# Kernel optimization log

Measured on AMD Instinct MI355X. Metric: run time of the kernel, lower is better.

The kernel has to match this reference:

```python
import jax, jax.numpy as jnp
import numpy as np

N, E, D = 50000, 300000, 64
EPS = 0.0  # eps buffer, train_eps=False


def setup_inputs() -> dict:
    key = jax.random.key(0)
    ks = jax.random.split(key, 24)
    inp = {}
    i = 0
    for d in range(3):
        inp[f"x{d}"] = jax.random.normal(ks[i], (N, D), jnp.float32); i += 1
        inp[f"up_index{d}"] = jax.random.randint(ks[i], (2, E), 0, N, jnp.int32); i += 1
        inp[f"down_index{d}"] = jax.random.randint(ks[i], (2, E), 0, N, jnp.int32); i += 1
        inp[f"up_attr{d}"] = jax.random.normal(ks[i], (E, D), jnp.float32); i += 1
        inp[f"down_attr{d}"] = jax.random.normal(ks[i], (E, D), jnp.float32); i += 1
    s2 = 1.0 / np.sqrt(2 * D)
    s1 = 1.0 / np.sqrt(D)
    inp["W_up"] = jax.random.normal(ks[i], (2 * D, D), jnp.float32) * s2; i += 1
    inp["b_up"] = jnp.zeros((D,), jnp.float32)
    inp["W_down"] = jax.random.normal(ks[i], (2 * D, D), jnp.float32) * s2; i += 1
    inp["b_down"] = jnp.zeros((D,), jnp.float32)
    inp["W1"] = jax.random.normal(ks[i], (D, D), jnp.float32) * s1; i += 1
    inp["b1"] = jnp.zeros((D,), jnp.float32)
    inp["W2"] = jax.random.normal(ks[i], (D, D), jnp.float32) * s1; i += 1
    inp["b2"] = jnp.zeros((D,), jnp.float32)
    return inp


def _level(x, up_idx, down_idx, up_attr, down_attr,
           W_up, b_up, W_down, b_down, W1, b1, W2, b2):
    # message_up: gather source feats, concat attr, MLP, scatter-add to targets
    m_up = jax.nn.relu(jnp.concatenate([x[up_idx[1]], up_attr], axis=-1) @ W_up + b_up)
    out_up = jax.ops.segment_sum(m_up, up_idx[0], num_segments=N)
    m_dn = jax.nn.relu(jnp.concatenate([x[down_idx[1]], down_attr], axis=-1) @ W_down + b_down)
    out_dn = jax.ops.segment_sum(m_dn, down_idx[0], num_segments=N)
    # out_up += (1+eps)x; out_down += (1+eps)x; update(out_up + out_down)
    h = out_up + out_dn + (2.0 * (1.0 + EPS)) * x
    return jax.nn.relu(jax.nn.relu(h @ W1 + b1) @ W2 + b2)


def reference(x0, up_index0, down_index0, up_attr0, down_attr0,
              x1, up_index1, down_index1, up_attr1, down_attr1,
              x2, up_index2, down_index2, up_attr2, down_attr2,
              W_up, b_up, W_down, b_down, W1, b1, W2, b2):
    params = (W_up, b_up, W_down, b_down, W1, b1, W2, b2)
    o0 = _level(x0, up_index0, down_index0, up_attr0, down_attr0, *params)
    o1 = _level(x1, up_index1, down_index1, up_attr1, down_attr1, *params)
    o2 = _level(x2, up_index2, down_index2, up_attr2, down_attr2, *params)
    return (o0, o1, o2)
```

## Files before the change

### kernel.cpp

```cpp
#include <hip/hip_runtime.h>
#include <hip/hip_fp16.h>

#define NN 50000
#define NE 300000
#define ETILES (NE / 16)
#define NTILES (NN / 16)

typedef _Float16 f16;
typedef _Float16 f16x4 __attribute__((ext_vector_type(4)));
typedef _Float16 f16x8 __attribute__((ext_vector_type(8)));
typedef float f32x4 __attribute__((ext_vector_type(4)));

__device__ __forceinline__ f16x4 cvt4(float4 v) {
    f16x4 r; r.x = (f16)v.x; r.y = (f16)v.y; r.z = (f16)v.z; r.w = (f16)v.w;
    return r;
}

__global__ void init2_kernel(const float* __restrict__ x0, const float* __restrict__ x1,
                             const float* __restrict__ x2,
                             f16* __restrict__ hbase, f16* __restrict__ xhbase) {
    const size_t i = (size_t)blockIdx.x * 256 + threadIdx.x;
    const int lvl = (int)(i / (NN * 16));
    const size_t li = i - (size_t)lvl * (NN * 16);
    const float* xs = (lvl == 0) ? x0 : (lvl == 1) ? x1 : x2;
    float4 v = ((const float4*)xs)[li];
    f16x4 xo, ho;
    xo.x = (f16)v.x;        xo.y = (f16)v.y;        xo.z = (f16)v.z;        xo.w = (f16)v.w;
    ho.x = (f16)(2.f*v.x);  ho.y = (f16)(2.f*v.y);  ho.z = (f16)(2.f*v.z);  ho.w = (f16)(2.f*v.w);
    ((f16x4*)(xhbase + (size_t)lvl * NN * 64))[li] = xo;
    ((f16x4*)(hbase  + (size_t)lvl * NN * 64))[li] = ho;
}

__global__ void initf32_kernel(const float* __restrict__ x0, const float* __restrict__ x1,
                               const float* __restrict__ x2, float* __restrict__ hbase) {
    const size_t i = (size_t)blockIdx.x * 256 + threadIdx.x;
    const int lvl = (int)(i / (NN * 16));
    const size_t li = i - (size_t)lvl * (NN * 16);
    const float* xs = (lvl == 0) ? x0 : (lvl == 1) ? x1 : x2;
    float4 v = ((const float4*)xs)[li];
    ((float4*)(hbase + (size_t)lvl * NN * 64))[li] =
        make_float4(2.f * v.x, 2.f * v.y, 2.f * v.z, 2.f * v.w);
}

__global__ void wtrans_kernel(const float* __restrict__ WU, const float* __restrict__ WD,
                              f16* __restrict__ WtU, f16* __restrict__ WtD) {
    const int i = blockIdx.x * 256 + threadIdx.x;
    const int k = i >> 6, c = i & 63;
    WtU[c * 128 + k] = (f16)WU[i];
    WtD[c * 128 + k] = (f16)WD[i];
}

#define WLDS_STRIDE 136

__device__ __forceinline__ int ld_comb(const int* __restrict__ idx, int tile, int l5) {
    const int e0 = tile << 4;
    return idx[(l5 < 16) ? (NE + e0 + l5) : (e0 + l5 - 16)];
}

__global__ __launch_bounds__(256) void edge4_kernel(
    const f16* __restrict__ xh,
    const int* __restrict__ ui, const int* __restrict__ di,
    const float* __restrict__ ua, const float* __restrict__ da,
    const f16* __restrict__ WtU, const f16* __restrict__ WtD,
    const float* __restrict__ bU, const float* __restrict__ bD,
    __half* __restrict__ h) {

    __shared__ __align__(16) f16 Wlds[64 * WLDS_STRIDE];

    const int dir = blockIdx.y;
    const int* __restrict__ idx    = dir ? di : ui;
    const float* __restrict__ attr = dir ? da : ua;
    const f16* __restrict__ Wt     = dir ? WtD : WtU;
    const float* __restrict__ b    = dir ? bD : bU;

    const int tt   = threadIdx.x;
    const int lane = tt & 63;
    const int wid  = tt >> 6;
    const int lr   = lane & 15;
    const int lg   = (lane >> 4) & 3;
    const int l5   = lane & 31;

    for (int i = tt; i < 1024; i += 256) {
        const int row = i >> 4, seg = i & 15;
        *(f16x8*)&Wlds[row * WLDS_STRIDE + seg * 8] = *(const f16x8*)&Wt[row * 128 + seg * 8];
    }
    float bf[4];
#pragma unroll
    for (int n = 0; n < 4; ++n) bf[n] = b[n * 16 + lr];
    __syncthreads();

    const float4* a4 = (const float4*)attr;

    const int S = gridDim.x * 4;
    int t = blockIdx.x * 4 + wid;
    if (t >= ETILES) return;

    int cB;
    int srcT, tgT[4];
    f16x4 gx[4];
    float4 pA[4];
    {
        const int cA = ld_comb(idx, t, l5);
        const int tn1 = t + S;
        cB = ld_comb(idx, (tn1 < ETILES) ? tn1 : t, l5);
        srcT = __shfl(cA, lr);
#pragma unroll
        for (int j = 0; j < 4; ++j) tgT[j] = __shfl(cA, 16 + 4 * lg + j);
        const int e0 = t << 4;
#pragma unroll
        for (int k0 = 0; k0 < 4; ++k0)
            gx[k0] = *(const f16x4*)&xh[(size_t)srcT * 64 + k0 * 16 + 4 * lg];
#pragma unroll
        for (int k0 = 0; k0 < 4; ++k0)
            pA[k0] = a4[(size_t)(e0 + lr) * 16 + 4 * k0 + lg];
    }

    for (; t < ETILES; t += S) {
        const int tn  = t + S;
        const int tnn = tn + S;

        const int srcN = __shfl(cB, lr);
        int tgN[4];
#pragma unroll
        for (int j = 0; j < 4; ++j) tgN[j] = __shfl(cB, 16 + 4 * lg + j);
        const int cC = ld_comb(idx, (tnn < ETILES) ? tnn : t, l5);

        const int tnc   = (tn < ETILES) ? tn : t;
        const int srcNc = (tn < ETILES) ? srcN : srcT;
        f16x4 gxN[4];
        float4 pAN[4];
        {
            const int e0n = tnc << 4;
#pragma unroll
            for (int k0 = 0; k0 < 4; ++k0)
                gxN[k0] = *(const f16x4*)&xh[(size_t)srcNc * 64 + k0 * 16 + 4 * lg];
#pragma unroll
            for (int k0 = 0; k0 < 4; ++k0)
                pAN[k0] = a4[(size_t)(e0n + lr) * 16 + 4 * k0 + lg];
        }

        f16x4 afr[8];
#pragma unroll
        for (int k0 = 0; k0 < 4; ++k0) afr[k0] = gx[k0];
#pragma unroll
        for (int k0 = 0; k0 < 4; ++k0) afr[4 + k0] = cvt4(pA[k0]);

        f32x4 acc[4];
#pragma unroll
        for (int n = 0; n < 4; ++n) acc[n] = (f32x4){0.f, 0.f, 0.f, 0.f};
#pragma unroll
        for (int k0 = 0; k0 < 8; ++k0) {
#pragma unroll
            for (int n = 0; n < 4; ++n) {
                const f16x4 wf = *(const f16x4*)&Wlds[(n * 16 + lr) * WLDS_STRIDE + k0 * 16 + 4 * lg];
                acc[n] = __builtin_amdgcn_mfma_f32_16x16x16f16(afr[k0], wf, acc[n], 0, 0, 0);
            }
        }

#pragma unroll
        for (int j = 0; j < 4; ++j) {
            float v[4], vn[4];
#pragma unroll
            for (int n = 0; n < 4; ++n) v[n] = fmaxf(acc[n][j] + bf[n], 0.f);
#pragma unroll
            for (int n = 0; n < 4; ++n) vn[n] = __shfl_xor(v[n], 1);
            __half* hp = h + (size_t)tgT[j] * 64;
            if ((lane & 1) == 0) {
                unsafeAtomicAdd((__half2*)(hp + 0 * 16 + lr), __floats2half2_rn(v[0], vn[0]));
                unsafeAtomicAdd((__half2*)(hp + 1 * 16 + lr), __floats2half2_rn(v[1], vn[1]));
            } else {
                unsafeAtomicAdd((__half2*)(hp + 2 * 16 + lr - 1), __floats2half2_rn(vn[2], v[2]));
                unsafeAtomicAdd((__half2*)(hp + 3 * 16 + lr - 1), __floats2half2_rn(vn[3], v[3]));
            }
        }

        srcT = srcN;
#pragma unroll
        for (int j = 0; j < 4; ++j) tgT[j] = tgN[j];
#pragma unroll
        for (int k0 = 0; k0 < 4; ++k0) { gx[k0] = gxN[k0]; pA[k0] = pAN[k0]; }
        cB = cC;
    }
}

__global__ __launch_bounds__(256) void edge_f32_kernel(
    const float* __restrict__ x, const int* __restrict__ idx,
    const float* __restrict__ attr, const float* __restrict__ W,
    const float* __restrict__ b, float* __restrict__ h) {

    const int t    = threadIdx.x;
    const int lane = t & 63;
    const int wid  = t >> 6;
    const int lr   = lane & 15;
    const int lg   = (lane >> 4) & 3;

    f16x4 wf[8][4];
#pragma unroll
    for (int k0 = 0; k0 < 8; ++k0) {
        const int kb = k0 * 16 + 4 * lg;
#pragma unroll
        for (int n = 0; n < 4; ++n) {
            const int c = n * 16 + lr;
            f16x4 w;
            w.x = (f16)W[(kb + 0) * 64 + c];
            w.y = (f16)W[(kb + 1) * 64 + c];
            w.z = (f16)W[(kb + 2) * 64 + c];
            w.w = (f16)W[(kb + 3) * 64 + c];
            wf[k0][n] = w;
        }
    }
    float bf[4];
#pragma unroll
    for (int n = 0; n < 4; ++n) bf[n] = b[n * 16 + lr];

    const float4* x4 = (const float4*)x;
    const float4* a4 = (const float4*)attr;

    const int gw     = blockIdx.x * 4 + wid;
    const int stride = gridDim.x * 4;
    for (int tile = gw; tile < ETILES; tile += stride) {
        const int e0  = tile << 4;
        const int src = idx[NE + e0 + lr];
        int tg[4];
#pragma unroll
        for (int j = 0; j < 4; ++j) tg[j] = idx[e0 + 4 * lg + j];

        f16x4 a[8];
#pragma unroll
        for (int k0 = 0; k0 < 4; ++k0)
            a[k0] = cvt4(x4[(size_t)src * 16 + 4 * k0 + lg]);
#pragma unroll
        for (int k0 = 0; k0 < 4; ++k0)
            a[4 + k0] = cvt4(a4[(size_t)(e0 + lr) * 16 + 4 * k0 + lg]);

        f32x4 acc[4];
#pragma unroll
        for (int n = 0; n < 4; ++n) acc[n] = (f32x4){0.f, 0.f, 0.f, 0.f};
#pragma unroll
        for (int k0 = 0; k0 < 8; ++k0)
#pragma unroll
            for (int n = 0; n < 4; ++n)
                acc[n] = __builtin_amdgcn_mfma_f32_16x16x16f16(a[k0], wf[k0][n], acc[n], 0, 0, 0);

#pragma unroll
        for (int j = 0; j < 4; ++j) {
            float* hp = h + (size_t)tg[j] * 64;
#pragma unroll
            for (int n = 0; n < 4; ++n) {
                float v = fmaxf(acc[n][j] + bf[n], 0.f);
                unsafeAtomicAdd(hp + n * 16 + lr, v);
            }
        }
    }
}

template<bool HALF>
__global__ __launch_bounds__(256) void node_kernel(
    const void* __restrict__ hbase, float* __restrict__ outb,
    const float* __restrict__ W1, const float* __restrict__ b1,
    const float* __restrict__ W2, const float* __restrict__ b2) {

    __shared__ f16 Y[4][16 * 72];

    const int t    = threadIdx.x;
    const int lane = t & 63;
    const int wid  = t >> 6;
    const int lr   = lane & 15;
    const int lg   = (lane >> 4) & 3;

    f16x4 w1f[4][4], w2f[4][4];
#pragma unroll
    for (int k0 = 0; k0 < 4; ++k0) {
        const int kb = k0 * 16 + 4 * lg;
#pragma unroll
        for (int n = 0; n < 4; ++n) {
            const int c = n * 16 + lr;
            f16x4 w;
            w.x = (f16)W1[(kb + 0) * 64 + c];
            w.y = (f16)W1[(kb + 1) * 64 + c];
            w.z = (f16)W1[(kb + 2) * 64 + c];
            w.w = (f16)W1[(kb + 3) * 64 + c];
            w1f[k0][n] = w;
            w.x = (f16)W2[(kb + 0) * 64 + c];
            w.y = (f16)W2[(kb + 1) * 64 + c];
            w.z = (f16)W2[(kb + 2) * 64 + c];
            w.w = (f16)W2[(kb + 3) * 64 + c];
            w2f[k0][n] = w;
        }
    }
    float b1f[4], b2f[4];
#pragma unroll
    for (int n = 0; n < 4; ++n) {
        b1f[n] = b1[n * 16 + lr];
        b2f[n] = b2[n * 16 + lr];
    }

    const int gw     = blockIdx.x * 4 + wid;
    const int stride = gridDim.x * 4;
    for (int tile = gw; tile < 3 * NTILES; tile += stride) {
        const int lvl = tile / NTILES;
        const int n0  = (tile - lvl * NTILES) << 4;
        float* out = outb + (size_t)lvl * NN * 64;

        f16x4 a[4];
        if (HALF) {
            const f16* h16 = (const f16*)hbase + (size_t)lvl * NN * 64;
#pragma unroll
            for (int k0 = 0; k0 < 4; ++k0)
                a[k0] = *(const f16x4*)&h16[(size_t)(n0 + lr) * 64 + k0 * 16 + 4 * lg];
        } else {
            const float4* h4 = (const float4*)((const float*)hbase + (size_t)lvl * NN * 64);
#pragma unroll
            for (int k0 = 0; k0 < 4; ++k0)
                a[k0] = cvt4(h4[(size_t)(n0 + lr) * 16 + 4 * k0 + lg]);
        }

        f32x4 acc[4];
#pragma unroll
        for (int n = 0; n < 4; ++n) acc[n] = (f32x4){0.f, 0.f, 0.f, 0.f};
#pragma unroll
        for (int k0 = 0; k0 < 4; ++k0)
#pragma unroll
            for (int n = 0; n < 4; ++n)
                acc[n] = __builtin_amdgcn_mfma_f32_16x16x16f16(a[k0], w1f[k0][n], acc[n], 0, 0, 0);

#pragma unroll
        for (int n = 0; n < 4; ++n)
#pragma unroll
            for (int j = 0; j < 4; ++j) {
                float v = acc[n][j] + b1f[n];
                v = v > 0.f ? v : 0.f;
                Y[wid][(4 * lg + j) * 72 + n * 16 + lr] = (f16)v;
            }

        f16x4 a2[4];
#pragma unroll
        for (int k0 = 0; k0 < 4; ++k0)
            a2[k0] = *(const f16x4*)&Y[wid][lr * 72 + k0 * 16 + 4 * lg];

        f32x4 acc2[4];
#pragma unroll
        for (int n = 0; n < 4; ++n) acc2[n] = (f32x4){0.f, 0.f, 0.f, 0.f};
#pragma unroll
        for (int k0 = 0; k0 < 4; ++k0)
#pragma unroll
            for (int n = 0; n < 4; ++n)
                acc2[n] = __builtin_amdgcn_mfma_f32_16x16x16f16(a2[k0], w2f[k0][n], acc2[n], 0, 0, 0);

#pragma unroll
        for (int n = 0; n < 4; ++n)
#pragma unroll
            for (int j = 0; j < 4; ++j) {
                float v = acc2[n][j] + b2f[n];
                v = v > 0.f ? v : 0.f;
                out[(size_t)(n0 + 4 * lg + j) * 64 + n * 16 + lr] = v;
            }
    }
}

extern "C" void kernel_launch(void* const* d_in, const int* in_sizes, int n_in,
                              void* d_out, int out_size, void* d_ws, size_t ws_size,
                              hipStream_t stream) {
    (void)in_sizes; (void)n_in; (void)out_size;

    const float* W_up   = (const float*)d_in[15];
    const float* b_up   = (const float*)d_in[16];
    const float* W_down = (const float*)d_in[17];
    const float* b_down = (const float*)d_in[18];
    const float* W1     = (const float*)d_in[19];
    const float* b1     = (const float*)d_in[20];
    const float* W2     = (const float*)d_in[21];
    const float* b2     = (const float*)d_in[22];

    const float* x0 = (const float*)d_in[0];
    const float* x1 = (const float*)d_in[5];
    const float* x2 = (const float*)d_in[10];

    const size_t hbytes  = (size_t)3 * NN * 64 * sizeof(f16);
    const size_t need    = 2 * hbytes + (size_t)2 * 128 * 64 * sizeof(f16);

    if (ws_size >= need) {
        f16* hbase  = (f16*)d_ws;
        f16* xhbase = hbase + (size_t)3 * NN * 64;
        f16* WtU    = (f16*)((char*)d_ws + 2 * hbytes);
        f16* WtD    = WtU + 128 * 64;

        wtrans_kernel<<<32, 256, 0, stream>>>(W_up, W_down, WtU, WtD);
        init2_kernel<<<9375, 256, 0, stream>>>(x0, x1, x2, hbase, xhbase);
        for (int d = 0; d < 3; ++d) {
            const int*   ui = (const int*)  d_in[5 * d + 1];
            const int*   di = (const int*)  d_in[5 * d + 2];
            const float* ua = (const float*)d_in[5 * d + 3];
            const float* da = (const float*)d_in[5 * d + 4];
            const f16* xh = xhbase + (size_t)d * NN * 64;
            __half* h = (__half*)(hbase + (size_t)d * NN * 64);
            edge4_kernel<<<dim3(1024, 2), 256, 0, stream>>>(
                xh, ui, di, ua, da, WtU, WtD, b_up, b_down, h);
        }
        node_kernel<true><<<586, 256, 0, stream>>>(hbase, (float*)d_out, W1, b1, W2, b2);
    } else {
        float* hbase = (float*)d_out;
        initf32_kernel<<<9375, 256, 0, stream>>>(x0, x1, x2, hbase);
        for (int d = 0; d < 3; ++d) {
            const float* x  = (const float*)d_in[5 * d + 0];
            const int*   ui = (const int*)  d_in[5 * d + 1];
            const int*   di = (const int*)  d_in[5 * d + 2];
            const float* ua = (const float*)d_in[5 * d + 3];
            const float* da = (const float*)d_in[5 * d + 4];
            float* h = hbase + (size_t)d * NN * 64;
            edge_f32_kernel<<<1024, 256, 0, stream>>>(x, ui, ua, W_up,   b_up,   h);
            edge_f32_kernel<<<1024, 256, 0, stream>>>(x, di, da, W_down, b_down, h);
        }
        node_kernel<false><<<586, 256, 0, stream>>>(hbase, (float*)d_out, W1, b1, W2, b2);
    }
}
```

Before: 433.8 us.

## Bucket edges by target and fuse edge messages with node MLP in LDS

Adds a counting-sort pass (histogram, scan, scatter of edge ids) that groups edges into 128-node target buckets. A single fused kernel per bucket and level computes both up and down messages with MFMA, accumulates them with fp32 LDS atomics instead of global half2 atomics, and then applies the two-layer node MLP directly from LDS. This removes the global fp16 aggregation buffer round trip and the global atomic traffic, at the cost of extra sort kernels, indirect gathers of attr rows through edge ids, and possible load imbalance across buckets. The old fp32 fallback path is dropped and the old edge4 kernel loses its software prefetch.

```diff
diff --git a/kernel.cpp b/kernel.cpp
--- a/kernel.cpp
+++ b/kernel.cpp
@@ -5,15 +5,34 @@
 #define NE 300000
 #define ETILES (NE / 16)
 #define NTILES (NN / 16)
+#define WLDS_STRIDE 136
+#define BKT 128
+#define NB 391
+#define NB1 392
+#define NCH 74
+#define CHSZ 4096
+#define HSTR 68
 
 typedef _Float16 f16;
 typedef _Float16 f16x4 __attribute__((ext_vector_type(4)));
-typedef _Float16 f16x8 __attribute__((ext_vector_type(8)));
 typedef float f32x4 __attribute__((ext_vector_type(4)));
+
+struct Idx6 { const int* p[6]; };
+struct FA { const float* x[3]; const int* idx[6]; const float* attr[6]; };
 
 __device__ __forceinline__ f16x4 cvt4(float4 v) {
     f16x4 r; r.x = (f16)v.x; r.y = (f16)v.y; r.z = (f16)v.z; r.w = (f16)v.w;
     return r;
+}
+
+__global__ void init_xh_kernel(const float* __restrict__ x0, const float* __restrict__ x1,
+                               const float* __restrict__ x2, f16* __restrict__ xhbase) {
+    const size_t i = (size_t)blockIdx.x * 256 + threadIdx.x;
+    const int lvl = (int)(i / (NN * 16));
+    const size_t li = i - (size_t)lvl * (NN * 16);
+    const float* xs = (lvl == 0) ? x0 : (lvl == 1) ? x1 : x2;
+    float4 v = ((const float4*)xs)[li];
+    ((f16x4*)(xhbase + (size_t)lvl * NN * 64))[li] = cvt4(v);
 }
 
 __global__ void init2_kernel(const float* __restrict__ x0, const float* __restrict__ x1,
@@ -31,17 +50,6 @@
     ((f16x4*)(hbase  + (size_t)lvl * NN * 64))[li] = ho;
 }
 
-__global__ void initf32_kernel(const float* __restrict__ x0, const float* __restrict__ x1,
-                               const float* __restrict__ x2, float* __restrict__ hbase) {
-    const size_t i = (size_t)blockIdx.x * 256 + threadIdx.x;
-    const int lvl = (int)(i / (NN * 16));
-    const size_t li = i - (size_t)lvl * (NN * 16);
-    const float* xs = (lvl == 0) ? x0 : (lvl == 1) ? x1 : x2;
-    float4 v = ((const float4*)xs)[li];
-    ((float4*)(hbase + (size_t)lvl * NN * 64))[li] =
-        make_float4(2.f * v.x, 2.f * v.y, 2.f * v.z, 2.f * v.w);
-}
-
 __global__ void wtrans_kernel(const float* __restrict__ WU, const float* __restrict__ WD,
                               f16* __restrict__ WtU, f16* __restrict__ WtD) {
     const int i = blockIdx.x * 256 + threadIdx.x;
@@ -50,7 +58,260 @@
     WtD[c * 128 + k] = (f16)WD[i];
 }
 
-#define WLDS_STRIDE 136
+__global__ void w12trans_kernel(const float* __restrict__ W1, const float* __restrict__ W2,
+                                f16* __restrict__ W1t, f16* __restrict__ W2t) {
+    const int i = blockIdx.x * 256 + threadIdx.x;
+    const int k = i >> 6, c = i & 63;
+    W1t[c * 64 + k] = (f16)W1[i];
+    W2t[c * 64 + k] = (f16)W2[i];
+}
+
+__global__ void hist_b_kernel(Idx6 idx, int* __restrict__ cntBC) {
+    __shared__ int c[NB];
+    const int t = threadIdx.x, ch = blockIdx.x, d = blockIdx.y;
+    for (int i = t; i < NB; i += 256) c[i] = 0;
+    __syncthreads();
+    const int base = ch * CHSZ;
+    const int* tg = idx.p[d];
+#pragma unroll
+    for (int i = 0; i < 16; ++i) {
+        const int e = base + i * 256 + t;
+        if (e < NE) atomicAdd(&c[tg[e] >> 7], 1);
+    }
+    __syncthreads();
+    for (int i = t; i < NB; i += 256) cntBC[(d * NB + i) * NCH + ch] = c[i];
+}
+
+__global__ void scan_b_kernel(const int* __restrict__ cntBC, int* __restrict__ offBC,
+                              int* __restrict__ rowptrB) {
+    __shared__ int sb[512];
+    const int t = threadIdx.x, d = blockIdx.x;
+    int tot = 0;
+    if (t < NB)
+        for (int c = 0; c < NCH; ++c) tot += cntBC[(d * NB + t) * NCH + c];
+    sb[t] = tot; __syncthreads();
+#pragma unroll
+    for (int off = 1; off < 512; off <<= 1) {
+        int v = (t >= off) ? sb[t - off] : 0;
+        __syncthreads();
+        sb[t] += v;
+        __syncthreads();
+    }
+    const int excl = sb[t] - tot;
+    if (t < NB) {
+        rowptrB[d * NB1 + t] = excl;
+        int run = excl;
+        for (int c = 0; c < NCH; ++c) {
+            offBC[(d * NB + t) * NCH + c] = run;
+            run += cntBC[(d * NB + t) * NCH + c];
+        }
+        if (t == NB - 1) rowptrB[d * NB1 + NB] = run;
+    }
+}
+
+__global__ void write_eids_b_kernel(Idx6 idx, const int* __restrict__ offBC,
+                                    int* __restrict__ eids) {
+    __shared__ int cur[NB];
+    const int t = threadIdx.x, ch = blockIdx.x, d = blockIdx.y;
+    for (int i = t; i < NB; i += 256) cur[i] = offBC[(d * NB + i) * NCH + ch];
+    __syncthreads();
+    const int base = ch * CHSZ;
+    const int* tg = idx.p[d];
+#pragma unroll
+    for (int i = 0; i < 16; ++i) {
+        const int e = base + i * 256 + t;
+        if (e < NE) {
+            const int p = atomicAdd(&cur[tg[e] >> 7], 1);
+            eids[(size_t)d * NE + p] = e;
+        }
+    }
+}
+
+__global__ __launch_bounds__(512) void fused_kernel(
+    FA fa, const f16* __restrict__ xhbase,
+    const f16* __restrict__ WtU, const f16* __restrict__ WtD,
+    const float* __restrict__ bU, const float* __restrict__ bD,
+    const int* __restrict__ eids, const int* __restrict__ rowptrB,
+    const f16* __restrict__ W1t, const f16* __restrict__ W2t,
+    const float* __restrict__ b1, const float* __restrict__ b2,
+    float* __restrict__ outb) {
+
+    __shared__ float hl[BKT * HSTR];
+    __shared__ f16 Y[8][16 * 72];
+
+    const int lvl  = blockIdx.y;
+    const int bkt  = blockIdx.x;
+    const int base = bkt * BKT;
+    const int tid  = threadIdx.x;
+    const int lane = tid & 63;
+    const int w    = tid >> 6;
+    const int lr   = lane & 15;
+    const int lg   = (lane >> 4) & 3;
+
+    const float* x  = fa.x[lvl];
+    const f16*   xh = xhbase + (size_t)lvl * NN * 64;
+    float*       out = outb + (size_t)lvl * NN * 64;
+
+    for (int i = tid; i < BKT * 16; i += 512) {
+        const int nl = i >> 4, c4 = i & 15;
+        float4 v = make_float4(0.f, 0.f, 0.f, 0.f);
+        if (base + nl < NN) v = ((const float4*)x)[(size_t)(base + nl) * 16 + c4];
+        ((float4*)&hl[nl * HSTR])[c4] = make_float4(2.f*v.x, 2.f*v.y, 2.f*v.z, 2.f*v.w);
+    }
+    __syncthreads();
+
+    for (int dir = 0; dir < 2; ++dir) {
+        const int d = 2 * lvl + dir;
+        const int* __restrict__ gidx  = fa.idx[d];
+        const float4* __restrict__ a4 = (const float4*)fa.attr[d];
+        const f16* __restrict__ Wt    = dir ? WtD : WtU;
+        const float* __restrict__ bb  = dir ? bD : bU;
+        const int* __restrict__ eid   = eids + (size_t)d * NE;
+        const int s0 = rowptrB[d * NB1 + bkt];
+        const int s1 = rowptrB[d * NB1 + bkt + 1];
+        if (s1 <= s0) continue;
+        const int T = (s1 - s0 + 15) >> 4;
+
+        f16x4 wf[8][4];
+#pragma unroll
+        for (int k0 = 0; k0 < 8; ++k0)
+#pragma unroll
+            for (int n = 0; n < 4; ++n)
+                wf[k0][n] = *(const f16x4*)&Wt[(n * 16 + lr) * 128 + k0 * 16 + 4 * lg];
+        float bf[4];
+#pragma unroll
+        for (int n = 0; n < 4; ++n) bf[n] = bb[n * 16 + lr];
+
+        if (w < T) {
+            int eA, sA, gA, gB;
+            float4 aB[4]; f16x4 xB[4];
+            {
+                const int sb = s0 + w * 16;
+                const int sl = (sb + lr < s1 - 1) ? (sb + lr) : (s1 - 1);
+                eA = eid[sl]; sA = gidx[NE + eA]; gA = gidx[eA];
+            }
+            {
+#pragma unroll
+                for (int k0 = 0; k0 < 4; ++k0) aB[k0] = a4[(size_t)eA * 16 + 4 * k0 + lg];
+#pragma unroll
+                for (int k0 = 0; k0 < 4; ++k0)
+                    xB[k0] = *(const f16x4*)&xh[(size_t)sA * 64 + k0 * 16 + 4 * lg];
+                gB = gA;
+            }
+            {
+                const int t2 = (w + 8 < T) ? (w + 8) : w;
+                const int sb = s0 + t2 * 16;
+                const int sl = (sb + lr < s1 - 1) ? (sb + lr) : (s1 - 1);
+                eA = eid[sl]; sA = gidx[NE + eA]; gA = gidx[eA];
+            }
+            for (int t = w; t < T; t += 8) {
+                float4 aN[4]; f16x4 xN[4]; const int gN = gA;
+#pragma unroll
+                for (int k0 = 0; k0 < 4; ++k0) aN[k0] = a4[(size_t)eA * 16 + 4 * k0 + lg];
+#pragma unroll
+                for (int k0 = 0; k0 < 4; ++k0)
+                    xN[k0] = *(const f16x4*)&xh[(size_t)sA * 64 + k0 * 16 + 4 * lg];
+                {
+                    const int t2 = (t + 16 < T) ? (t + 16) : t;
+                    const int sb = s0 + t2 * 16;
+                    const int sl = (sb + lr < s1 - 1) ? (sb + lr) : (s1 - 1);
+                    eA = eid[sl]; sA = gidx[NE + eA]; gA = gidx[eA];
+                }
+                {
+                    const int sb = s0 + t * 16;
+                    f16x4 afr[8];
+#pragma unroll
+                    for (int k0 = 0; k0 < 4; ++k0) afr[k0] = xB[k0];
+#pragma unroll
+                    for (int k0 = 0; k0 < 4; ++k0) afr[4 + k0] = cvt4(aB[k0]);
+                    f32x4 acc[4];
+#pragma unroll
+                    for (int n = 0; n < 4; ++n) acc[n] = (f32x4){0.f, 0.f, 0.f, 0.f};
+#pragma unroll
+                    for (int k0 = 0; k0 < 8; ++k0)
+#pragma unroll
+                        for (int n = 0; n < 4; ++n)
+                            acc[n] = __builtin_amdgcn_mfma_f32_16x16x16f16(afr[k0], wf[k0][n], acc[n], 0, 0, 0);
+#pragma unroll
+                    for (int j = 0; j < 4; ++j) {
+                        const int row = 4 * lg + j;
+                        const int nl  = __shfl(gB, row) - base;
+                        const bool ok = (sb + row) < s1;
+#pragma unroll
+                        for (int n = 0; n < 4; ++n) {
+                            const float v = fmaxf(acc[n][j] + bf[n], 0.f);
+                            if (ok) atomicAdd(&hl[nl * HSTR + n * 16 + lr], v);
+                        }
+                    }
+                }
+#pragma unroll
+                for (int k0 = 0; k0 < 4; ++k0) { aB[k0] = aN[k0]; xB[k0] = xN[k0]; }
+                gB = gN;
+            }
+        }
+    }
+    __syncthreads();
+
+    f16x4 w1f[4][4], w2f[4][4];
+#pragma unroll
+    for (int k0 = 0; k0 < 4; ++k0)
+#pragma unroll
+        for (int n = 0; n < 4; ++n) {
+            w1f[k0][n] = *(const f16x4*)&W1t[(n * 16 + lr) * 64 + k0 * 16 + 4 * lg];
+            w2f[k0][n] = *(const f16x4*)&W2t[(n * 16 + lr) * 64 + k0 * 16 + 4 * lg];
+        }
+    float b1f[4], b2f[4];
+#pragma unroll
+    for (int n = 0; n < 4; ++n) { b1f[n] = b1[n * 16 + lr]; b2f[n] = b2[n * 16 + lr]; }
+
+    const int r0 = w * 16;
+    f16x4 a[4];
+#pragma unroll
+    for (int k0 = 0; k0 < 4; ++k0) {
+        f16x4 tv;
+#pragma unroll
+        for (int jj = 0; jj < 4; ++jj)
+            tv[jj] = (f16)hl[(r0 + lr) * HSTR + k0 * 16 + 4 * lg + jj];
+        a[k0] = tv;
+    }
+    f32x4 acc[4];
+#pragma unroll
+    for (int n = 0; n < 4; ++n) acc[n] = (f32x4){0.f, 0.f, 0.f, 0.f};
+#pragma unroll
+    for (int k0 = 0; k0 < 4; ++k0)
+#pragma unroll
+        for (int n = 0; n < 4; ++n)
+            acc[n] = __builtin_amdgcn_mfma_f32_16x16x16f16(a[k0], w1f[k0][n], acc[n], 0, 0, 0);
+#pragma unroll
+    for (int n = 0; n < 4; ++n)
+#pragma unroll
+        for (int j = 0; j < 4; ++j) {
+            float v = acc[n][j] + b1f[n];
+            v = v > 0.f ? v : 0.f;
+            Y[w][(4 * lg + j) * 72 + n * 16 + lr] = (f16)v;
+        }
+    f16x4 a2[4];
+#pragma unroll
+    for (int k0 = 0; k0 < 4; ++k0)
+        a2[k0] = *(const f16x4*)&Y[w][lr * 72 + k0 * 16 + 4 * lg];
+    f32x4 acc2[4];
+#pragma unroll
+    for (int n = 0; n < 4; ++n) acc2[n] = (f32x4){0.f, 0.f, 0.f, 0.f};
+#pragma unroll
+    for (int k0 = 0; k0 < 4; ++k0)
+#pragma unroll
+        for (int n = 0; n < 4; ++n)
+            acc2[n] = __builtin_amdgcn_mfma_f32_16x16x16f16(a2[k0], w2f[k0][n], acc2[n], 0, 0, 0);
+#pragma unroll
+    for (int n = 0; n < 4; ++n)
+#pragma unroll
+        for (int j = 0; j < 4; ++j) {
+            const int node = base + r0 + 4 * lg + j;
+            float v = acc2[n][j] + b2f[n];
+            v = v > 0.f ? v : 0.f;
+            if (node < NN) out[(size_t)node * 64 + n * 16 + lr] = v;
+        }
+}
 
 __device__ __forceinline__ int ld_comb(const int* __restrict__ idx, int tile, int l5) {
     const int e0 = tile << 4;
@@ -80,9 +341,9 @@
     const int lg   = (lane >> 4) & 3;
     const int l5   = lane & 31;
 
-    for (int i = tt; i < 1024; i += 256) {
-        const int row = i >> 4, seg = i & 15;
-        *(f16x8*)&Wlds[row * WLDS_STRIDE + seg * 8] = *(const f16x8*)&Wt[row * 128 + seg * 8];
+    for (int i = tt; i < 2048; i += 256) {
+        const int row = i >> 5, seg = i & 31;
+        *(f16x4*)&Wlds[row * WLDS_STRIDE + seg * 4] = *(const f16x4*)&Wt[row * 128 + seg * 4];
     }
     float bf[4];
 #pragma unroll
@@ -90,72 +351,36 @@
     __syncthreads();
 
     const float4* a4 = (const float4*)attr;
-
     const int S = gridDim.x * 4;
     int t = blockIdx.x * 4 + wid;
     if (t >= ETILES) return;
 
-    int cB;
-    int srcT, tgT[4];
-    f16x4 gx[4];
-    float4 pA[4];
-    {
+    for (; t < ETILES; t += S) {
+        const int e0 = t << 4;
         const int cA = ld_comb(idx, t, l5);
-        const int tn1 = t + S;
-        cB = ld_comb(idx, (tn1 < ETILES) ? tn1 : t, l5);
-        srcT = __shfl(cA, lr);
-#pragma unroll
-        for (int j = 0; j < 4; ++j) tgT[j] = __shfl(cA, 16 + 4 * lg + j);
-        const int e0 = t << 4;
+        const int src = __shfl(cA, lr);
+        int tg[4];
+#pragma unroll
+        for (int j = 0; j < 4; ++j) tg[j] = __shfl(cA, 16 + 4 * lg + j);
+
+        f16x4 afr[8];
 #pragma unroll
         for (int k0 = 0; k0 < 4; ++k0)
-            gx[k0] = *(const f16x4*)&xh[(size_t)srcT * 64 + k0 * 16 + 4 * lg];
+            afr[k0] = *(const f16x4*)&xh[(size_t)src * 64 + k0 * 16 + 4 * lg];
 #pragma unroll
         for (int k0 = 0; k0 < 4; ++k0)
-            pA[k0] = a4[(size_t)(e0 + lr) * 16 + 4 * k0 + lg];
-    }
-
-    for (; t < ETILES; t += S) {
-        const int tn  = t + S;
-        const int tnn = tn + S;
-
-        const int srcN = __shfl(cB, lr);
-        int tgN[4];
-#pragma unroll
-        for (int j = 0; j < 4; ++j) tgN[j] = __shfl(cB, 16 + 4 * lg + j);
-        const int cC = ld_comb(idx, (tnn < ETILES) ? tnn : t, l5);
-
-        const int tnc   = (tn < ETILES) ? tn : t;
-        const int srcNc = (tn < ETILES) ? srcN : srcT;
-        f16x4 gxN[4];
-        float4 pAN[4];
-        {
-            const int e0n = tnc << 4;
-#pragma unroll
-            for (int k0 = 0; k0 < 4; ++k0)
-                gxN[k0] = *(const f16x4*)&xh[(size_t)srcNc * 64 + k0 * 16 + 4 * lg];
-#pragma unroll
-            for (int k0 = 0; k0 < 4; ++k0)
-                pAN[k0] = a4[(size_t)(e0n + lr) * 16 + 4 * k0 + lg];
-        }
-
-        f16x4 afr[8];
-#pragma unroll
-        for (int k0 = 0; k0 < 4; ++k0) afr[k0] = gx[k0];
-#pragma unroll
-        for (int k0 = 0; k0 < 4; ++k0) afr[4 + k0] = cvt4(pA[k0]);
+            afr[4 + k0] = cvt4(a4[(size_t)(e0 + lr) * 16 + 4 * k0 + lg]);
 
         f32x4 acc[4];
 #pragma unroll
-        for (int n = 0; n < 4; ++n) acc[n] = (f32x4){0.f, 0.f, 0.f, 0.f};
-#pragma unroll
-        for (int k0 = 0; k0 < 8; ++k0) {
+        for (int n = 0; n < 4; ++n) acc[n] = (f32x4){0, 0, 0, 0};
+#pragma unroll
+        for (int k0 = 0; k0 < 8; ++k0)
 #pragma unroll
             for (int n = 0; n < 4; ++n) {
-                const f16x4 wf = *(const f16x4*)&Wlds[(n * 16 + lr) * WLDS_STRIDE + k0 * 16 + 4 * lg];
-                acc[n] = __builtin_amdgcn_mfma_f32_16x16x16f16(afr[k0], wf, acc[n], 0, 0, 0);
-            }
-        }
+                const f16x4 wfv = *(const f16x4*)&Wlds[(n * 16 + lr) * WLDS_STRIDE + k0 * 16 + 4 * lg];
+                acc[n] = __builtin_amdgcn_mfma_f32_16x16x16f16(afr[k0], wfv, acc[n], 0, 0, 0);
+            }
 
 #pragma unroll
         for (int j = 0; j < 4; ++j) {
@@ -164,7 +389,7 @@
             for (int n = 0; n < 4; ++n) v[n] = fmaxf(acc[n][j] + bf[n], 0.f);
 #pragma unroll
             for (int n = 0; n < 4; ++n) vn[n] = __shfl_xor(v[n], 1);
-            __half* hp = h + (size_t)tgT[j] * 64;
+            __half* hp = h + (size_t)tg[j] * 64;
             if ((lane & 1) == 0) {
                 unsafeAtomicAdd((__half2*)(hp + 0 * 16 + lr), __floats2half2_rn(v[0], vn[0]));
                 unsafeAtomicAdd((__half2*)(hp + 1 * 16 + lr), __floats2half2_rn(v[1], vn[1]));
@@ -173,20 +398,15 @@
                 unsafeAtomicAdd((__half2*)(hp + 3 * 16 + lr - 1), __floats2half2_rn(vn[3], v[3]));
             }
         }
-
-        srcT = srcN;
-#pragma unroll
-        for (int j = 0; j < 4; ++j) tgT[j] = tgN[j];
-#pragma unroll
-        for (int k0 = 0; k0 < 4; ++k0) { gx[k0] = gxN[k0]; pA[k0] = pAN[k0]; }
-        cB = cC;
-    }
-}
-
-__global__ __launch_bounds__(256) void edge_f32_kernel(
-    const float* __restrict__ x, const int* __restrict__ idx,
-    const float* __restrict__ attr, const float* __restrict__ W,
-    const float* __restrict__ b, float* __restrict__ h) {
+    }
+}
+
+__global__ __launch_bounds__(256) void node_kernel(
+    const f16* __restrict__ hbase, float* __restrict__ outb,
+    const float* __restrict__ W1, const float* __restrict__ b1,
+    const float* __restrict__ W2, const float* __restrict__ b2) {
+
+    __shared__ f16 Y[4][16 * 72];
 
     const int t    = threadIdx.x;
     const int lane = t & 63;
@@ -194,98 +414,24 @@
     const int lr   = lane & 15;
     const int lg   = (lane >> 4) & 3;
 
-    f16x4 wf[8][4];
-#pragma unroll
-    for (int k0 = 0; k0 < 8; ++k0) {
+    f16x4 w1f[4][4], w2f[4][4];
+#pragma unroll
+    for (int k0 = 0; k0 < 4; ++k0) {
         const int kb = k0 * 16 + 4 * lg;
 #pragma unroll
         for (int n = 0; n < 4; ++n) {
             const int c = n * 16 + lr;
-            f16x4 w;
-            w.x = (f16)W[(kb + 0) * 64 + c];
-            w.y = (f16)W[(kb + 1) * 64 + c];
-            w.z = (f16)W[(kb + 2) * 64 + c];
-            w.w = (f16)W[(kb + 3) * 64 + c];
-            wf[k0][n] = w;
-        }
-    }
-    float bf[4];
-#pragma unroll
-    for (int n = 0; n < 4; ++n) bf[n] = b[n * 16 + lr];
-
-    const float4* x4 = (const float4*)x;
-    const float4* a4 = (const float4*)attr;
-
-    const int gw     = blockIdx.x * 4 + wid;
-    const int stride = gridDim.x * 4;
-    for (int tile = gw; tile < ETILES; tile += stride) {
-        const int e0  = tile << 4;
-        const int src = idx[NE + e0 + lr];
-        int tg[4];
-#pragma unroll
-        for (int j = 0; j < 4; ++j) tg[j] = idx[e0 + 4 * lg + j];
-
-        f16x4 a[8];
-#pragma unroll
-        for (int k0 = 0; k0 < 4; ++k0)
-            a[k0] = cvt4(x4[(size_t)src * 16 + 4 * k0 + lg]);
-#pragma unroll
-        for (int k0 = 0; k0 < 4; ++k0)
-            a[4 + k0] = cvt4(a4[(size_t)(e0 + lr) * 16 + 4 * k0 + lg]);
-
-        f32x4 acc[4];
-#pragma unroll
-        for (int n = 0; n < 4; ++n) acc[n] = (f32x4){0.f, 0.f, 0.f, 0.f};
-#pragma unroll
-        for (int k0 = 0; k0 < 8; ++k0)
-#pragma unroll
-            for (int n = 0; n < 4; ++n)
-                acc[n] = __builtin_amdgcn_mfma_f32_16x16x16f16(a[k0], wf[k0][n], acc[n], 0, 0, 0);
-
-#pragma unroll
-        for (int j = 0; j < 4; ++j) {
-            float* hp = h + (size_t)tg[j] * 64;
-#pragma unroll
-            for (int n = 0; n < 4; ++n) {
-                float v = fmaxf(acc[n][j] + bf[n], 0.f);
-                unsafeAtomicAdd(hp + n * 16 + lr, v);
-            }
-        }
-    }
-}
-
-template<bool HALF>
-__global__ __launch_bounds__(256) void node_kernel(
-    const void* __restrict__ hbase, float* __restrict__ outb,
-    const float* __restrict__ W1, const float* __restrict__ b1,
-    const float* __restrict__ W2, const float* __restrict__ b2) {
-
-    __shared__ f16 Y[4][16 * 72];
-
-    const int t    = threadIdx.x;
-    const int lane = t & 63;
-    const int wid  = t >> 6;
-    const int lr   = lane & 15;
-    const int lg   = (lane >> 4) & 3;
-
-    f16x4 w1f[4][4], w2f[4][4];
-#pragma unroll
-    for (int k0 = 0; k0 < 4; ++k0) {
-        const int kb = k0 * 16 + 4 * lg;
-#pragma unroll
-        for (int n = 0; n < 4; ++n) {
-            const int c = n * 16 + lr;
-            f16x4 w;
-            w.x = (f16)W1[(kb + 0) * 64 + c];
-            w.y = (f16)W1[(kb + 1) * 64 + c];
-            w.z = (f16)W1[(kb + 2) * 64 + c];
-            w.w = (f16)W1[(kb + 3) * 64 + c];
-            w1f[k0][n] = w;
-            w.x = (f16)W2[(kb + 0) * 64 + c];
-            w.y = (f16)W2[(kb + 1) * 64 + c];
-            w.z = (f16)W2[(kb + 2) * 64 + c];
-            w.w = (f16)W2[(kb + 3) * 64 + c];
-            w2f[k0][n] = w;
+            f16x4 wv;
+            wv.x = (f16)W1[(kb + 0) * 64 + c];
+            wv.y = (f16)W1[(kb + 1) * 64 + c];
+            wv.z = (f16)W1[(kb + 2) * 64 + c];
+            wv.w = (f16)W1[(kb + 3) * 64 + c];
+            w1f[k0][n] = wv;
+            wv.x = (f16)W2[(kb + 0) * 64 + c];
+            wv.y = (f16)W2[(kb + 1) * 64 + c];
+            wv.z = (f16)W2[(kb + 2) * 64 + c];
+            wv.w = (f16)W2[(kb + 3) * 64 + c];
+            w2f[k0][n] = wv;
         }
     }
     float b1f[4], b2f[4];
@@ -301,23 +447,16 @@
         const int lvl = tile / NTILES;
         const int n0  = (tile - lvl * NTILES) << 4;
         float* out = outb + (size_t)lvl * NN * 64;
+        const f16* h16 = hbase + (size_t)lvl * NN * 64;
 
         f16x4 a[4];
-        if (HALF) {
-            const f16* h16 = (const f16*)hbase + (size_t)lvl * NN * 64;
-#pragma unroll
-            for (int k0 = 0; k0 < 4; ++k0)
-                a[k0] = *(const f16x4*)&h16[(size_t)(n0 + lr) * 64 + k0 * 16 + 4 * lg];
-        } else {
-            const float4* h4 = (const float4*)((const float*)hbase + (size_t)lvl * NN * 64);
-#pragma unroll
-            for (int k0 = 0; k0 < 4; ++k0)
-                a[k0] = cvt4(h4[(size_t)(n0 + lr) * 16 + 4 * k0 + lg]);
-        }
+#pragma unroll
+        for (int k0 = 0; k0 < 4; ++k0)
+            a[k0] = *(const f16x4*)&h16[(size_t)(n0 + lr) * 64 + k0 * 16 + 4 * lg];
 
         f32x4 acc[4];
 #pragma unroll
-        for (int n = 0; n < 4; ++n) acc[n] = (f32x4){0.f, 0.f, 0.f, 0.f};
+        for (int n = 0; n < 4; ++n) acc[n] = (f32x4){0, 0, 0, 0};
 #pragma unroll
         for (int k0 = 0; k0 < 4; ++k0)
 #pragma unroll
@@ -340,7 +479,7 @@
 
         f32x4 acc2[4];
 #pragma unroll
-        for (int n = 0; n < 4; ++n) acc2[n] = (f32x4){0.f, 0.f, 0.f, 0.f};
+        for (int n = 0; n < 4; ++n) acc2[n] = (f32x4){0, 0, 0, 0};
 #pragma unroll
         for (int k0 = 0; k0 < 4; ++k0)
 #pragma unroll
@@ -376,41 +515,67 @@
     const float* x1 = (const float*)d_in[5];
     const float* x2 = (const float*)d_in[10];
 
-    const size_t hbytes  = (size_t)3 * NN * 64 * sizeof(f16);
-    const size_t need    = 2 * hbytes + (size_t)2 * 128 * 64 * sizeof(f16);
-
-    if (ws_size >= need) {
-        f16* hbase  = (f16*)d_ws;
-        f16* xhbase = hbase + (size_t)3 * NN * 64;
-        f16* WtU    = (f16*)((char*)d_ws + 2 * hbytes);
-        f16* WtD    = WtU + 128 * 64;
+    size_t off = 0;
+    auto alloc = [&](size_t bytes) { size_t o = off; off = (off + bytes + 255) & ~(size_t)255; return o; };
+    const size_t o_xh    = alloc((size_t)3 * NN * 64 * 2);
+    const size_t o_agg   = alloc((size_t)3 * NN * 64 * 2);
+    const size_t o_wt    = alloc((size_t)2 * 128 * 64 * 2);
+    const size_t fallback_need = off;
+    const size_t o_w12   = alloc((size_t)2 * 64 * 64 * 2);
+    const size_t o_cnt   = alloc((size_t)6 * NB * NCH * 4);
+    const size_t o_off   = alloc((size_t)6 * NB * NCH * 4);
+    const size_t o_rpB   = alloc((size_t)6 * NB1 * 4);
+    const size_t o_eid   = alloc((size_t)6 * NE * 4);
+    const size_t full_need = off;
+
+    char* ws = (char*)d_ws;
+    f16* xh  = (f16*)(ws + o_xh);
+    f16* agg = (f16*)(ws + o_agg);
+    f16* WtU = (f16*)(ws + o_wt);
+    f16* WtD = WtU + 128 * 64;
+
+    Idx6 idx;
+    FA fa;
+    for (int d = 0; d < 3; ++d) {
+        fa.x[d] = (const float*)d_in[5 * d + 0];
+        idx.p[2 * d + 0] = fa.idx[2 * d + 0] = (const int*)d_in[5 * d + 1];
+        idx.p[2 * d + 1] = fa.idx[2 * d + 1] = (const int*)d_in[5 * d + 2];
+        fa.attr[2 * d + 0] = (const float*)d_in[5 * d + 3];
+        fa.attr[2 * d + 1] = (const float*)d_in[5 * d + 4];
+    }
+
+    if (ws_size >= full_need) {
+        f16* W1t = (f16*)(ws + o_w12);
+        f16* W2t = W1t + 64 * 64;
+        int* cntBC   = (int*)(ws + o_cnt);
+        int* offBC   = (int*)(ws + o_off);
+        int* rowptrB = (int*)(ws + o_rpB);
+        int* eids    = (int*)(ws + o_eid);
 
         wtrans_kernel<<<32, 256, 0, stream>>>(W_up, W_down, WtU, WtD);
-        init2_kernel<<<9375, 256, 0, stream>>>(x0, x1, x2, hbase, xhbase);
+        w12trans_kernel<<<16, 256, 0, stream>>>(W1, W2, W1t, W2t);
+        init_xh_kernel<<<9375, 256, 0, stream>>>(x0, x1, x2, xh);
+
+        hist_b_kernel<<<dim3(NCH, 6), 256, 0, stream>>>(idx, cntBC);
+        scan_b_kernel<<<6, 512, 0, stream>>>(cntBC, offBC, rowptrB);
+        write_eids_b_kernel<<<dim3(NCH, 6), 256, 0, stream>>>(idx, offBC, eids);
+
+        fused_kernel<<<dim3(NB, 3), 512, 0, stream>>>(
+            fa, xh, WtU, WtD, b_up, b_down, eids, rowptrB,
+            W1t, W2t, b1, b2, (float*)d_out);
+    } else if (ws_size >= fallback_need) {
+        wtrans_kernel<<<32, 256, 0, stream>>>(W_up, W_down, WtU, WtD);
+        init2_kernel<<<9375, 256, 0, stream>>>(x0, x1, x2, agg, xh);
         for (int d = 0; d < 3; ++d) {
             const int*   ui = (const int*)  d_in[5 * d + 1];
             const int*   di = (const int*)  d_in[5 * d + 2];
             const float* ua = (const float*)d_in[5 * d + 3];
             const float* da = (const float*)d_in[5 * d + 4];
-            const f16* xh = xhbase + (size_t)d * NN * 64;
-            __half* h = (__half*)(hbase + (size_t)d * NN * 64);
+            const f16* xhd = xh + (size_t)d * NN * 64;
+            __half* h = (__half*)(agg + (size_t)d * NN * 64);
             edge4_kernel<<<dim3(1024, 2), 256, 0, stream>>>(
-                xh, ui, di, ua, da, WtU, WtD, b_up, b_down, h);
-        }
-        node_kernel<true><<<586, 256, 0, stream>>>(hbase, (float*)d_out, W1, b1, W2, b2);
-    } else {
-        float* hbase = (float*)d_out;
-        initf32_kernel<<<9375, 256, 0, stream>>>(x0, x1, x2, hbase);
-        for (int d = 0; d < 3; ++d) {
-            const float* x  = (const float*)d_in[5 * d + 0];
-            const int*   ui = (const int*)  d_in[5 * d + 1];
-            const int*   di = (const int*)  d_in[5 * d + 2];
-            const float* ua = (const float*)d_in[5 * d + 3];
-            const float* da = (const float*)d_in[5 * d + 4];
-            float* h = hbase + (size_t)d * NN * 64;
-            edge_f32_kernel<<<1024, 256, 0, stream>>>(x, ui, ua, W_up,   b_up,   h);
-            edge_f32_kernel<<<1024, 256, 0, stream>>>(x, di, da, W_down, b_down, h);
-        }
-        node_kernel<false><<<586, 256, 0, stream>>>(hbase, (float*)d_out, W1, b1, W2, b2);
-    }
-}
+                xhd, ui, di, ua, da, WtU, WtD, b_up, b_down, h);
+        }
+        node_kernel<<<586, 256, 0, stream>>>(agg, (float*)d_out, W1, b1, W2, b2);
+    }
+}
```

Measured after the change: 805.4 us. 85.7% more time.
